# Kernel optimization log

Hardware: AMD Instinct MI355X
Metric: run time of the kernel (lower is better)

The kernel has to match this reference:

```python
import jax, jax.numpy as jnp
import numpy as np

# ---- constants matching init opt ----
SQRT_FRAGS = 8
N_PATCH = SQRT_FRAGS * SQRT_FRAGS  # 64
TH1_INIT = 0.85
PATCH_MEAN = 0.1
MORPH = 5          # morphology_size (odd -> same-size pooling)
STEP = 5e-5
FRAME_PATCHES = np.array([0, 1, 2, 3, 4, 5, 6, 7, 8, 15, 16, 23, 24, 31, 32, 39,
                          40, 47, 48, 55, 56, 57, 58, 59, 60, 61, 62, 63])
H = W = 3072


def setup_inputs() -> dict:
    key = jax.random.key(0)
    x = jax.random.uniform(key, (1, 1, H, W), dtype=jnp.float32)
    return {"x": x}


def _frac_above(p, th):
    # mean of where(p > th, 1, 0)
    return jnp.mean((p > th).astype(jnp.float32))


def _find_thresholds(patches):
    """Sequential per-patch threshold search with th1 carried across patches
    (faithful to the stateful self.th1 in the torch module).
    patches: (64, ph, pw). Returns per-patch final threshold (64,)."""
    f_bias = jnp.zeros((N_PATCH,), jnp.float32).at[jnp.asarray(FRAME_PATCHES)].set(0.05)

    def per_patch(th, inp):
        p, fb = inp
        lo_tgt = PATCH_MEAN + 0.02 - fb   # loop 1: while frac < lo_tgt: th -= STEP
        hi_tgt = PATCH_MEAN - 0.02 - fb   # loop 2: while frac > hi_tgt: th += STEP
        th = jax.lax.while_loop(lambda t: _frac_above(p, t) < lo_tgt,
                                lambda t: t - STEP, th)
        th = jax.lax.while_loop(lambda t: _frac_above(p, t) > hi_tgt,
                                lambda t: t + STEP, th)
        return th, th

    _, ths = jax.lax.scan(per_patch, jnp.float32(TH1_INIT), (patches, f_bias))
    return ths


def _maxpool(x, k=MORPH):
    # PyTorch MaxPool2d(k, stride=1, padding=k//2) pads with -inf -> same size
    pad = k // 2
    return jax.lax.reduce_window(
        x, -jnp.inf, jax.lax.max,
        window_dimensions=(1, 1, k, k), window_strides=(1, 1, 1, 1),
        padding=[(0, 0), (0, 0), (pad, pad), (pad, pad)])


def reference(x):
    N, c, h, w = x.shape
    ph, pw = h // SQRT_FRAGS, w // SQRT_FRAGS
    # unfold with kernel=stride=ph -> non-overlapping patches, row-major order
    patches = (x[0, 0]
               .reshape(SQRT_FRAGS, ph, SQRT_FRAGS, pw)
               .transpose(0, 2, 1, 3)
               .reshape(N_PATCH, ph, pw))
    ths = _find_thresholds(patches)
    binary = (patches > ths[:, None, None]).astype(jnp.float32)
    # fold back to full image
    img = (binary
           .reshape(SQRT_FRAGS, SQRT_FRAGS, ph, pw)
           .transpose(0, 2, 1, 3)
           .reshape(1, 1, h, w))
    # morphological close: maxpool then minpool (minpool = -maxpool(-x))
    out = -_maxpool(-_maxpool(img))
    return out
```

## Files before the change

kernel.cpp:

```cpp
#include <hip/hip_runtime.h>
#include <stdint.h>

constexpr int IMG     = 3072;
constexpr int NPIX    = IMG * IMG;
constexpr int PH      = 384;
constexpr int NPATCH  = 64;
constexpr int NSLICE  = 8;
constexpr int SROWS   = PH / NSLICE;
constexpr int WPR     = IMG / 32;
constexpr int NWORDS  = NPIX / 32;
constexpr uint32_t KEY_LO = 0x3F000000u;
constexpr uint32_t KEY_HI = 0x3F800000u;
constexpr uint32_t STEPU = 839u;
constexpr uint32_t G0 = KEY_LO + 704u;
constexpr int NB = 9999;
constexpr int CH = (NB + 255) / 256;
constexpr int TR = 12;

constexpr size_t OFF_THS  = 0;
constexpr size_t OFF_HIST = 512;
constexpr size_t OFF_B    = OFF_HIST + (size_t)NPATCH * NB * 4;
constexpr int HIST_U32 = NPATCH * NB;
constexpr int HIST_U4  = HIST_U32 / 4;

__global__ __launch_bounds__(256) void k_zero(uint32_t* __restrict__ h) {
    int i = blockIdx.x * 256 + threadIdx.x;
    if (i < HIST_U4) {
        uint4 z = make_uint4(0u, 0u, 0u, 0u);
        *reinterpret_cast<uint4*>(h + (size_t)i * 4) = z;
    }
}

__global__ __launch_bounds__(256) void k_hist(const float* __restrict__ x,
                                              uint32_t* __restrict__ ph_hist) {
    __shared__ uint32_t hist[NB];
    const int p = blockIdx.x >> 3, s = blockIdx.x & 7;
    const int t = threadIdx.x;
    const int pr = p >> 3, pc = p & 7;
    const float* base = x + (size_t)(pr * PH + s * SROWS) * IMG + pc * PH;

    for (int i = t; i < NB; i += 256) hist[i] = 0;
    __syncthreads();

    constexpr int NF4 = SROWS * (PH / 4);
    for (int i = t; i < NF4; i += 256) {
        int r = i / 96, c = i - r * 96;
        float4 v = *reinterpret_cast<const float4*>(base + (size_t)r * IMG + c * 4);
        float vals[4] = {v.x, v.y, v.z, v.w};
#pragma unroll
        for (int k = 0; k < 4; ++k) {
            uint32_t key = __float_as_uint(vals[k]);
            if (key > G0) {
                uint32_t idx = (key - KEY_LO + 134u) / 839u;
                if (idx > (uint32_t)(NB - 1)) idx = NB - 1;
                atomicAdd(&hist[idx], 1u);
            }
        }
    }
    __syncthreads();
    uint32_t* out = ph_hist + (size_t)p * NB;
    for (int i = t; i < NB; i += 256) {
        uint32_t h = hist[i];
        if (h) atomicAdd(&out[i], h);
    }
}

__global__ __launch_bounds__(256) void k_scan(const uint32_t* __restrict__ ph_hist,
                                              float* __restrict__ ths) {
    __shared__ uint32_t h[NB];
    __shared__ uint32_t csum[256];
    __shared__ uint32_t after[256];
    __shared__ int best_s[256];
    const int p = blockIdx.x, t = threadIdx.x;
    const uint32_t* src = ph_hist + (size_t)p * NB;
    for (int i = t; i < NB; i += 256) h[i] = src[i];
    __syncthreads();

    const int lo = t * CH;
    const int hi = (lo + CH < NB) ? lo + CH : NB;
    uint32_t s = 0;
    for (int i = lo; i < hi; ++i) s += h[i];
    csum[t] = s;
    __syncthreads();
    if (t == 0) {
        uint32_t acc = 0;
        for (int u = 255; u >= 0; --u) { after[u] = acc; acc += csum[u]; }
    }
    __syncthreads();

    const int pr = p >> 3, pc = p & 7;
    const bool frame = (pr == 0 || pr == 7 || pc == 0 || pc == 7);
    const float hi_t = 0.08f - (frame ? 0.05f : 0.0f);
    int d = (int)((double)hi_t * 147456.0);
    while ((float)(d + 1) / 147456.0f <= hi_t) ++d;
    while (d > 0 && (float)d / 147456.0f > hi_t) --d;
    const uint32_t Chi = (uint32_t)d;

    uint32_t run = after[t];
    int best = 0x7FFFFFFF;
    for (int i = hi - 1; i >= lo; --i) {
        run += h[i];
        if (i >= 1 && run <= Chi) best = i;
    }
    best_s[t] = best;
    __syncthreads();
    for (int st = 128; st > 0; st >>= 1) {
        if (t < st) { int o = best_s[t + st]; if (o < best_s[t]) best_s[t] = o; }
        __syncthreads();
    }
    if (t == 0) {
        int istar = best_s[0];
        int j = (istar == 0x7FFFFFFF) ? (NB - 2) : (istar - 1);
        ths[p] = __uint_as_float(G0 + (uint32_t)j * STEPU);
    }
}

__global__ __launch_bounds__(256) void k_pack(const float* __restrict__ x,
                                              const float* __restrict__ ths,
                                              uint32_t* __restrict__ B) {
    __shared__ float ths_s[NPATCH];
    int t = threadIdx.x;
    if (t < NPATCH) ths_s[t] = ths[t];
    __syncthreads();
    int wi = blockIdx.x * 256 + t;
    if (wi >= NWORDS) return;
    int y  = wi / WPR;
    int wx = wi - y * WPR;
    float th = ths_s[(y / PH) * 8 + (wx * 32) / PH];
    const float* row = x + (size_t)y * IMG + wx * 32;
    uint32_t m = 0;
#pragma unroll
    for (int k = 0; k < 8; ++k) {
        float4 v = *reinterpret_cast<const float4*>(row + 4 * k);
        m |= (uint32_t)(v.x > th) << (4 * k + 0);
        m |= (uint32_t)(v.y > th) << (4 * k + 1);
        m |= (uint32_t)(v.z > th) << (4 * k + 2);
        m |= (uint32_t)(v.w > th) << (4 * k + 3);
    }
    B[wi] = m;
}

__device__ __forceinline__ uint32_t hshift5_or(uint32_t c, uint32_t l, uint32_t r) {
    uint64_t xr = ((uint64_t)r << 32) | c;
    uint64_t xl = ((uint64_t)c << 32) | l;
    return c | (uint32_t)(xr >> 1) | (uint32_t)(xr >> 2)
             | (uint32_t)(xl >> 31) | (uint32_t)(xl >> 30);
}
__device__ __forceinline__ uint32_t hshift5_and(uint32_t c, uint32_t l, uint32_t r) {
    uint64_t xr = ((uint64_t)r << 32) | c;
    uint64_t xl = ((uint64_t)c << 32) | l;
    return c & (uint32_t)(xr >> 1) & (uint32_t)(xr >> 2)
             & (uint32_t)(xl >> 31) & (uint32_t)(xl >> 30);
}

__global__ __launch_bounds__(256) void k_close_store(const uint32_t* __restrict__ B,
                                                     float* __restrict__ out) {
    __shared__ uint32_t Bs[TR + 8][WPR];
    __shared__ uint32_t Ds[TR + 4][WPR];
    const int y0 = blockIdx.x * TR;
    const int t = threadIdx.x;

    for (int i = t; i < (TR + 8) * WPR; i += 256) {
        int r = i / WPR, c = i - r * WPR;
        int gy = y0 - 4 + r;
        Bs[r][c] = (gy >= 0 && gy < IMG) ? B[gy * WPR + c] : 0u;
    }
    __syncthreads();

    for (int i = t; i < (TR + 4) * WPR; i += 256) {
        int r = i / WPR, c = i - r * WPR;
        uint32_t acc = 0;
#pragma unroll
        for (int dy = -2; dy <= 2; ++dy) {
            int br = r + 2 + dy;
            uint32_t cc = Bs[br][c];
            uint32_t ll = (c > 0)       ? Bs[br][c - 1] : 0u;
            uint32_t rr = (c < WPR - 1) ? Bs[br][c + 1] : 0u;
            acc |= hshift5_or(cc, ll, rr);
        }
        Ds[r][c] = acc;
    }
    __syncthreads();

    for (int i = t; i < TR * WPR; i += 256) {
        int r = i / WPR, c = i - r * WPR;
        int gy = y0 + r;
        uint32_t acc = 0xFFFFFFFFu;
#pragma unroll
        for (int dy = -2; dy <= 2; ++dy) {
            int yy = gy + dy;
            if (yy < 0 || yy >= IMG) continue;
            int dr = r + 2 + dy;
            uint32_t cc = Ds[dr][c];
            uint32_t ll = (c > 0)       ? Ds[dr][c - 1] : 0xFFFFFFFFu;
            uint32_t rr = (c < WPR - 1) ? Ds[dr][c + 1] : 0xFFFFFFFFu;
            acc &= hshift5_and(cc, ll, rr);
        }
        float* o = out + (size_t)gy * IMG + c * 32;
#pragma unroll
        for (int k = 0; k < 8; ++k) {
            float4 v;
            v.x = (acc & (1u << (4 * k + 0))) ? 1.0f : 0.0f;
            v.y = (acc & (1u << (4 * k + 1))) ? 1.0f : 0.0f;
            v.z = (acc & (1u << (4 * k + 2))) ? 1.0f : 0.0f;
            v.w = (acc & (1u << (4 * k + 3))) ? 1.0f : 0.0f;
            *reinterpret_cast<float4*>(o + 4 * k) = v;
        }
    }
}

extern "C" void kernel_launch(void* const* d_in, const int* in_sizes, int n_in,
                              void* d_out, int out_size, void* d_ws, size_t ws_size,
                              hipStream_t stream) {
    const float* x = (const float*)d_in[0];
    float* out = (float*)d_out;
    uint8_t* ws = (uint8_t*)d_ws;

    float*    ths  = (float*)(ws + OFF_THS);
    uint32_t* hist = (uint32_t*)(ws + OFF_HIST);
    uint32_t* Bb   = (uint32_t*)(ws + OFF_B);

    int gz = (HIST_U4 + 255) / 256;
    int gw = NWORDS / 256;

    k_zero <<<gz, 256, 0, stream>>>(hist);
    k_hist <<<NPATCH * NSLICE, 256, 0, stream>>>(x, hist);
    k_scan <<<NPATCH, 256, 0, stream>>>(hist, ths);
    k_pack <<<gw, 256, 0, stream>>>(x, ths, Bb);
    k_close_store<<<IMG / TR, 256, 0, stream>>>(Bb, out);
}
```

Measured before the change: 140.6 us.

## Fuse binarize into 2D-tiled close kernel and drop histogram zeroing

Two structural changes. Each histogram block now writes a private copy of its histogram without global atomics, and the scan kernel sums the eight slices, so the separate zeroing kernel disappears. The pack kernel and the bitmask buffer are removed: a new 2D-tiled close kernel thresholds the input directly into shared-memory bit words, including a halo, then runs the dilate and erode passes. This saves one launch and the bitmask round-trip through global memory, at the cost of re-reading halo pixels from the input in each tile and a larger private histogram buffer.

```diff
diff --git a/kernel.cpp b/kernel.cpp
--- a/kernel.cpp
+++ b/kernel.cpp
@@ -8,31 +8,26 @@
 constexpr int NSLICE  = 8;
 constexpr int SROWS   = PH / NSLICE;
 constexpr int WPR     = IMG / 32;
-constexpr int NWORDS  = NPIX / 32;
 constexpr uint32_t KEY_LO = 0x3F000000u;
-constexpr uint32_t KEY_HI = 0x3F800000u;
 constexpr uint32_t STEPU = 839u;
 constexpr uint32_t G0 = KEY_LO + 704u;
 constexpr int NB = 9999;
 constexpr int CH = (NB + 255) / 256;
-constexpr int TR = 12;
+
+constexpr int TR = 24;
+constexpr int TC = 24;
+constexpr int GR = IMG / TR;
+constexpr int GC = WPR / TC;
+constexpr int BROWS  = TR + 8;
+constexpr int BWORDS = TC + 4;
+constexpr int DROWS  = TR + 4;
+constexpr int DWORDS = TC + 2;
 
 constexpr size_t OFF_THS  = 0;
-constexpr size_t OFF_HIST = 512;
-constexpr size_t OFF_B    = OFF_HIST + (size_t)NPATCH * NB * 4;
-constexpr int HIST_U32 = NPATCH * NB;
-constexpr int HIST_U4  = HIST_U32 / 4;
-
-__global__ __launch_bounds__(256) void k_zero(uint32_t* __restrict__ h) {
-    int i = blockIdx.x * 256 + threadIdx.x;
-    if (i < HIST_U4) {
-        uint4 z = make_uint4(0u, 0u, 0u, 0u);
-        *reinterpret_cast<uint4*>(h + (size_t)i * 4) = z;
-    }
-}
+constexpr size_t OFF_PRIV = 512;
 
 __global__ __launch_bounds__(256) void k_hist(const float* __restrict__ x,
-                                              uint32_t* __restrict__ ph_hist) {
+                                              uint32_t* __restrict__ priv) {
     __shared__ uint32_t hist[NB];
     const int p = blockIdx.x >> 3, s = blockIdx.x & 7;
     const int t = threadIdx.x;
@@ -58,22 +53,24 @@
         }
     }
     __syncthreads();
-    uint32_t* out = ph_hist + (size_t)p * NB;
-    for (int i = t; i < NB; i += 256) {
-        uint32_t h = hist[i];
-        if (h) atomicAdd(&out[i], h);
-    }
-}
-
-__global__ __launch_bounds__(256) void k_scan(const uint32_t* __restrict__ ph_hist,
+    uint32_t* out = priv + (size_t)blockIdx.x * NB;
+    for (int i = t; i < NB; i += 256) out[i] = hist[i];
+}
+
+__global__ __launch_bounds__(256) void k_scan(const uint32_t* __restrict__ priv,
                                               float* __restrict__ ths) {
     __shared__ uint32_t h[NB];
     __shared__ uint32_t csum[256];
     __shared__ uint32_t after[256];
     __shared__ int best_s[256];
     const int p = blockIdx.x, t = threadIdx.x;
-    const uint32_t* src = ph_hist + (size_t)p * NB;
-    for (int i = t; i < NB; i += 256) h[i] = src[i];
+    for (int i = t; i < NB; i += 256) {
+        uint32_t sum = 0;
+#pragma unroll
+        for (int b = 0; b < NSLICE; ++b)
+            sum += priv[(size_t)(p * NSLICE + b) * NB + i];
+        h[i] = sum;
+    }
     __syncthreads();
 
     const int lo = t * CH;
@@ -115,31 +112,6 @@
     }
 }
 
-__global__ __launch_bounds__(256) void k_pack(const float* __restrict__ x,
-                                              const float* __restrict__ ths,
-                                              uint32_t* __restrict__ B) {
-    __shared__ float ths_s[NPATCH];
-    int t = threadIdx.x;
-    if (t < NPATCH) ths_s[t] = ths[t];
-    __syncthreads();
-    int wi = blockIdx.x * 256 + t;
-    if (wi >= NWORDS) return;
-    int y  = wi / WPR;
-    int wx = wi - y * WPR;
-    float th = ths_s[(y / PH) * 8 + (wx * 32) / PH];
-    const float* row = x + (size_t)y * IMG + wx * 32;
-    uint32_t m = 0;
-#pragma unroll
-    for (int k = 0; k < 8; ++k) {
-        float4 v = *reinterpret_cast<const float4*>(row + 4 * k);
-        m |= (uint32_t)(v.x > th) << (4 * k + 0);
-        m |= (uint32_t)(v.y > th) << (4 * k + 1);
-        m |= (uint32_t)(v.z > th) << (4 * k + 2);
-        m |= (uint32_t)(v.w > th) << (4 * k + 3);
-    }
-    B[wi] = m;
-}
-
 __device__ __forceinline__ uint32_t hshift5_or(uint32_t c, uint32_t l, uint32_t r) {
     uint64_t xr = ((uint64_t)r << 32) | c;
     uint64_t xl = ((uint64_t)c << 32) | l;
@@ -153,50 +125,73 @@
              & (uint32_t)(xl >> 31) & (uint32_t)(xl >> 30);
 }
 
-__global__ __launch_bounds__(256) void k_close_store(const uint32_t* __restrict__ B,
-                                                     float* __restrict__ out) {
-    __shared__ uint32_t Bs[TR + 8][WPR];
-    __shared__ uint32_t Ds[TR + 4][WPR];
-    const int y0 = blockIdx.x * TR;
+__global__ __launch_bounds__(256) void k_binclose(const float* __restrict__ x,
+                                                  const float* __restrict__ ths,
+                                                  float* __restrict__ out) {
+    __shared__ float    ths_s[NPATCH];
+    __shared__ uint32_t Bs[BROWS][BWORDS];
+    __shared__ uint32_t Ds[DROWS][DWORDS];
+    const int bid = blockIdx.x;
+    const int ry = bid / GC, cx = bid - ry * GC;
+    const int y0 = ry * TR;
+    const int w0 = cx * TC;
     const int t = threadIdx.x;
 
-    for (int i = t; i < (TR + 8) * WPR; i += 256) {
-        int r = i / WPR, c = i - r * WPR;
+    if (t < NPATCH) ths_s[t] = ths[t];
+    __syncthreads();
+
+    for (int i = t; i < BROWS * BWORDS; i += 256) {
+        int r = i / BWORDS, w = i - r * BWORDS;
         int gy = y0 - 4 + r;
-        Bs[r][c] = (gy >= 0 && gy < IMG) ? B[gy * WPR + c] : 0u;
-    }
-    __syncthreads();
-
-    for (int i = t; i < (TR + 4) * WPR; i += 256) {
-        int r = i / WPR, c = i - r * WPR;
+        int gw = w0 - 2 + w;
+        uint32_t m = 0;
+        if (gy >= 0 && gy < IMG && gw >= 0 && gw < WPR) {
+            float th = ths_s[(gy / PH) * 8 + gw / 12];
+            const float* row = x + (size_t)gy * IMG + gw * 32;
+#pragma unroll
+            for (int k = 0; k < 8; ++k) {
+                float4 v = *reinterpret_cast<const float4*>(row + 4 * k);
+                m |= (uint32_t)(v.x > th) << (4 * k + 0);
+                m |= (uint32_t)(v.y > th) << (4 * k + 1);
+                m |= (uint32_t)(v.z > th) << (4 * k + 2);
+                m |= (uint32_t)(v.w > th) << (4 * k + 3);
+            }
+        }
+        Bs[r][w] = m;
+    }
+    __syncthreads();
+
+    for (int i = t; i < DROWS * DWORDS; i += 256) {
+        int rd = i / DWORDS, wd = i - rd * DWORDS;
         uint32_t acc = 0;
 #pragma unroll
         for (int dy = -2; dy <= 2; ++dy) {
-            int br = r + 2 + dy;
-            uint32_t cc = Bs[br][c];
-            uint32_t ll = (c > 0)       ? Bs[br][c - 1] : 0u;
-            uint32_t rr = (c < WPR - 1) ? Bs[br][c + 1] : 0u;
+            int rb = rd + 2 + dy;
+            uint32_t cc = Bs[rb][wd + 1];
+            uint32_t ll = Bs[rb][wd];
+            uint32_t rr = Bs[rb][wd + 2];
             acc |= hshift5_or(cc, ll, rr);
         }
-        Ds[r][c] = acc;
-    }
-    __syncthreads();
-
-    for (int i = t; i < TR * WPR; i += 256) {
-        int r = i / WPR, c = i - r * WPR;
+        Ds[rd][wd] = acc;
+    }
+    __syncthreads();
+
+    for (int i = t; i < TR * TC; i += 256) {
+        int r = i / TC, w = i - r * TC;
         int gy = y0 + r;
+        int gw = w0 + w;
         uint32_t acc = 0xFFFFFFFFu;
 #pragma unroll
         for (int dy = -2; dy <= 2; ++dy) {
             int yy = gy + dy;
             if (yy < 0 || yy >= IMG) continue;
-            int dr = r + 2 + dy;
-            uint32_t cc = Ds[dr][c];
-            uint32_t ll = (c > 0)       ? Ds[dr][c - 1] : 0xFFFFFFFFu;
-            uint32_t rr = (c < WPR - 1) ? Ds[dr][c + 1] : 0xFFFFFFFFu;
+            int rd = r + 2 + dy;
+            uint32_t cc = Ds[rd][w + 1];
+            uint32_t ll = (gw > 0)       ? Ds[rd][w]     : 0xFFFFFFFFu;
+            uint32_t rr = (gw < WPR - 1) ? Ds[rd][w + 2] : 0xFFFFFFFFu;
             acc &= hshift5_and(cc, ll, rr);
         }
-        float* o = out + (size_t)gy * IMG + c * 32;
+        float* o = out + (size_t)gy * IMG + gw * 32;
 #pragma unroll
         for (int k = 0; k < 8; ++k) {
             float4 v;
@@ -217,15 +212,9 @@
     uint8_t* ws = (uint8_t*)d_ws;
 
     float*    ths  = (float*)(ws + OFF_THS);
-    uint32_t* hist = (uint32_t*)(ws + OFF_HIST);
-    uint32_t* Bb   = (uint32_t*)(ws + OFF_B);
-
-    int gz = (HIST_U4 + 255) / 256;
-    int gw = NWORDS / 256;
-
-    k_zero <<<gz, 256, 0, stream>>>(hist);
-    k_hist <<<NPATCH * NSLICE, 256, 0, stream>>>(x, hist);
-    k_scan <<<NPATCH, 256, 0, stream>>>(hist, ths);
-    k_pack <<<gw, 256, 0, stream>>>(x, ths, Bb);
-    k_close_store<<<IMG / TR, 256, 0, stream>>>(Bb, out);
-}
+    uint32_t* priv = (uint32_t*)(ws + OFF_PRIV);
+
+    k_hist    <<<NPATCH * NSLICE, 256, 0, stream>>>(x, priv);
+    k_scan    <<<NPATCH,          256, 0, stream>>>(priv, ths);
+    k_binclose<<<GR * GC,         256, 0, stream>>>(x, ths, out);
+}
```

Result: faster. 135.4 us (-3.7%).
